# Kernel tuning notes

Measured on AMD Instinct MI355X. Metric: run time of the kernel, lower is better.

The kernel has to match this reference:

```python
import jax, jax.numpy as jnp
import numpy as np

DIM = 1024
BATCH = 8
SEQ = 2048


def setup_inputs() -> dict:
    key = jax.random.key(0)
    ks = jax.random.split(key, 10)
    s = 0.02
    return {
        "x": jax.random.normal(ks[0], (BATCH, SEQ, DIM), dtype=jnp.float32),
        "Wq": jax.random.normal(ks[1], (DIM, DIM), dtype=jnp.float32) * s,
        "bq": jnp.zeros((DIM,), jnp.float32),
        "Wk": jax.random.normal(ks[2], (DIM, DIM), dtype=jnp.float32) * s,
        "bk": jnp.zeros((DIM,), jnp.float32),
        "Wv": jax.random.normal(ks[3], (DIM, DIM), dtype=jnp.float32) * s,
        "bv": jnp.zeros((DIM,), jnp.float32),
        "Wo": jax.random.normal(ks[4], (DIM, DIM), dtype=jnp.float32) * s,
        "bo": jnp.zeros((DIM,), jnp.float32),
        "decay_param": jnp.asarray(0.0, jnp.float32),
    }


def reference(x, Wq, bq, Wk, bk, Wv, bv, Wo, bo, decay_param):
    # projections: [B,S,D] @ [D,D]
    q = x @ Wq + bq
    k = jax.nn.elu(x @ Wk + bk) + 1.0  # F.elu(k) + 1.0
    v = x @ Wv + bv
    decay = jax.nn.sigmoid(decay_param)
    B, S, D = x.shape

    def step(mem, qkv):
        q_t, k_t, v_t = qkv  # each [B, D]
        # read BEFORE update (output at t uses memory from steps < t)
        read = jnp.einsum('bd,bde->be', q_t, mem)
        mem = decay * mem + k_t[:, :, None] * v_t[:, None, :]  # rank-1 outer product
        return mem, read

    mem0 = jnp.zeros((B, D, D), x.dtype)
    # scan over time: move seq axis to front
    _, outs = jax.lax.scan(
        step, mem0,
        (q.transpose(1, 0, 2), k.transpose(1, 0, 2), v.transpose(1, 0, 2)))
    out = outs.transpose(1, 0, 2)  # [B, S, D]
    return out @ Wo + bo
```

## Files before the change

kernel.cpp:

```cpp
#include <hip/hip_runtime.h>
#include <cstdint>
#include <cstddef>

typedef __bf16 bf16;
typedef __attribute__((ext_vector_type(8))) __bf16 bf16x8;
typedef __attribute__((ext_vector_type(4))) __bf16 bf16x4;
typedef __attribute__((ext_vector_type(4))) float f32x4;
typedef __attribute__((ext_vector_type(4))) int i32x4;

#define ADIM 1024
#define ASEQ 2048
#define ABATCH 8

__device__ __forceinline__ void gload_lds16(const void* g, void* l) {
  __builtin_amdgcn_global_load_lds(
      (const __attribute__((address_space(1))) void*)g,
      (__attribute__((address_space(3))) void*)l,
      16, 0, 0);
}

__device__ __forceinline__ f32x4 mfma16(bf16x8 a, bf16x8 b, f32x4 c) {
  return __builtin_amdgcn_mfma_f32_16x16x32_bf16(a, b, c, 0, 0, 0);
}
__device__ __forceinline__ i32x4 mfma8i(i32x4 a, i32x4 b, i32x4 c) {
  return __builtin_amdgcn_mfma_i32_16x16x64_i8(a, b, c, 0, 0, 0);
}

__global__ __launch_bounds__(256) void k_prep_w(
    const float* __restrict__ Wq, const float* __restrict__ Wk,
    const float* __restrict__ Wv, const float* __restrict__ Wo,
    bf16* __restrict__ WcT, bf16* __restrict__ WoT) {
  const int b = blockIdx.x;
  const int which = b >> 8, t = b & 255;
  const int n0 = (t & 15) * 64, k0 = (t >> 4) * 64;
  const float* W = (which == 0) ? Wq : (which == 1) ? Wk : (which == 2) ? Wv : Wo;
  bf16* out = (which < 3) ? (WcT + (size_t)which * ADIM * ADIM) : WoT;

  __shared__ float tile[64][69];
  const int r = threadIdx.x >> 4, c4 = (threadIdx.x & 15) * 4;
#pragma unroll
  for (int p = 0; p < 4; ++p) {
    float4 f = *(const float4*)&W[(size_t)(k0 + p * 16 + r) * ADIM + n0 + c4];
    tile[p * 16 + r][c4 + 0] = f.x;
    tile[p * 16 + r][c4 + 1] = f.y;
    tile[p * 16 + r][c4 + 2] = f.z;
    tile[p * 16 + r][c4 + 3] = f.w;
  }
  __syncthreads();
#pragma unroll
  for (int p = 0; p < 4; ++p) {
    const int nn = p * 16 + r;
    bf16x4 o;
#pragma unroll
    for (int j = 0; j < 4; ++j) o[j] = (bf16)tile[c4 + j][nn];
    *(bf16x4*)&out[(size_t)(n0 + nn) * ADIM + k0 + c4] = o;
  }
}

__global__ __launch_bounds__(256) void k_q(
    const float* __restrict__ x, const bf16* __restrict__ WcT,
    signed char* __restrict__ Xq, float* __restrict__ sx,
    signed char* __restrict__ WcQ, float* __restrict__ swc) {
  const int row = blockIdx.x * 4 + (threadIdx.x >> 6);
  const int l = threadIdx.x & 63;
  float v[16];
  if (row < 16384) {
    const float4* p = (const float4*)&x[(size_t)row * ADIM + l * 16];
#pragma unroll
    for (int g = 0; g < 4; ++g) {
      float4 f = p[g];
      v[g * 4 + 0] = f.x; v[g * 4 + 1] = f.y; v[g * 4 + 2] = f.z; v[g * 4 + 3] = f.w;
    }
  } else {
    const bf16x8* p = (const bf16x8*)&WcT[(size_t)(row - 16384) * ADIM + l * 16];
#pragma unroll
    for (int g = 0; g < 2; ++g) {
      bf16x8 f = p[g];
#pragma unroll
      for (int e = 0; e < 8; ++e) v[g * 8 + e] = (float)f[e];
    }
  }
  float m = 0.f;
#pragma unroll
  for (int e = 0; e < 16; ++e) m = fmaxf(m, fabsf(v[e]));
#pragma unroll
  for (int off = 32; off >= 1; off >>= 1) m = fmaxf(m, __shfl_xor(m, off));
  m = fmaxf(m, 1e-20f);
  const float inv = 127.f / m;
  i32x4 pk;
#pragma unroll
  for (int g = 0; g < 4; ++g) {
    int word = 0;
#pragma unroll
    for (int e = 0; e < 4; ++e) {
      int q = __float2int_rn(v[g * 4 + e] * inv);
      q = max(-127, min(127, q));
      word |= (q & 255) << (e * 8);
    }
    pk[g] = word;
  }
  if (row < 16384) {
    *(i32x4*)&Xq[(size_t)row * ADIM + l * 16] = pk;
    if (l == 0) sx[row] = m / 127.f;
  } else {
    *(i32x4*)&WcQ[(size_t)(row - 16384) * ADIM + l * 16] = pk;
    if (l == 0) swc[row - 16384] = m / 127.f;
  }
}

__global__ __launch_bounds__(512, 2) void k_qkv8(
    const signed char* __restrict__ A, const signed char* __restrict__ BT,
    const float* __restrict__ sx, const float* __restrict__ swc,
    const float* __restrict__ bias0, const float* __restrict__ bias1,
    const float* __restrict__ bias2,
    bf16* __restrict__ Qo, bf16* __restrict__ Ko, bf16* __restrict__ Vto)
{
  constexpr int K = 1024;
  constexpr int KT = 16;
  const int nwg = gridDim.x;
  const int cpx = nwg >> 3;
  const int flat = blockIdx.x;
  const int sw = (flat & 7) * cpx + (flat >> 3);
  const int bx = sw % 12, by = sw / 12;
  const int m0 = by * 256, n0 = bx * 256;

  const int tid = threadIdx.x;
  const int l = tid & 63, w = tid >> 6;
  const int wm = w >> 2, wn = w & 3;
  const int lr = l & 15, kg = l >> 4;

  __shared__ alignas(16) signed char sA[3][256 * 64];
  __shared__ alignas(16) signed char sB[3][256 * 64];

  i32x4 acc[8][4] = {};

  int oA[8], oB[4];
#pragma unroll
  for (int i = 0; i < 8; ++i) {
    int r = wm * 128 + i * 16 + lr;
    oA[i] = (r * 4 + (kg ^ (r & 3))) * 16;
  }
#pragma unroll
  for (int j = 0; j < 4; ++j) {
    int r = wn * 64 + j * 16 + lr;
    oB[j] = (r * 4 + (kg ^ (r & 3))) * 16;
  }

  auto stA = [&](int sp, int kt, int chunk) {
    int s = chunk * 512 + tid;
    int prow = s >> 2, ps = s & 3;
    int lc = ps ^ (prow & 3);
    gload_lds16(A + (size_t)(m0 + prow) * K + kt * 64 + lc * 16,
                &sA[sp][(size_t)s * 16]);
  };
  auto stB = [&](int sp, int kt, int chunk) {
    int s = chunk * 512 + tid;
    int prow = s >> 2, ps = s & 3;
    int lc = ps ^ (prow & 3);
    gload_lds16(BT + (size_t)(n0 + prow) * K + kt * 64 + lc * 16,
                &sB[sp][(size_t)s * 16]);
  };

#pragma unroll
  for (int tt = 0; tt < 2; ++tt) {
    stA(tt, tt, 0); stA(tt, tt, 1);
    stB(tt, tt, 0); stB(tt, tt, 1);
  }
  asm volatile("s_waitcnt vmcnt(4)\n\ts_barrier" ::: "memory");

  for (int t = 0; t < KT; ++t) {
    const int s = t % 3;
    const char* bA = (const char*)&sA[s][0];
    const char* bB = (const char*)&sB[s][0];

    i32x4 af[8], bfr[4];
#pragma unroll
    for (int i = 0; i < 8; ++i) af[i] = *(const i32x4*)(bA + oA[i]);
#pragma unroll
    for (int j = 0; j < 4; ++j) bfr[j] = *(const i32x4*)(bB + oB[j]);

    const int tp = (t + 2 < KT) ? t + 2 : t;
    stA((t + 2) % 3, tp, 0); stA((t + 2) % 3, tp, 1);
    stB((t + 2) % 3, tp, 0); stB((t + 2) % 3, tp, 1);

    __builtin_amdgcn_s_setprio(1);
#pragma unroll
    for (int i = 0; i < 8; ++i)
#pragma unroll
      for (int j = 0; j < 4; ++j)
        acc[i][j] = mfma8i(af[i], bfr[j], acc[i][j]);
    __builtin_amdgcn_s_setprio(0);

    asm volatile("s_waitcnt vmcnt(4)\n\ts_barrier" ::: "memory");
  }
  asm volatile("s_waitcnt vmcnt(0)" ::: "memory");

  const int cb = n0 >> 10;
#pragma unroll
  for (int i = 0; i < 8; ++i) {
#pragma unroll
    for (int jj = 0; jj < 4; ++jj) {
      const int n = n0 + wn * 64 + jj * 16 + lr;
      const int m0r = m0 + wm * 128 + i * 16 + kg * 4;
      const int nn = n & 1023;
      const float swn = swc[n];
      const float4 s4 = *(const float4*)&sx[m0r];
      float de[4];
      de[0] = (float)acc[i][jj][0] * s4.x * swn;
      de[1] = (float)acc[i][jj][1] * s4.y * swn;
      de[2] = (float)acc[i][jj][2] * s4.z * swn;
      de[3] = (float)acc[i][jj][3] * s4.w * swn;
      if (cb == 0) {
        const float b_ = bias0[nn];
#pragma unroll
        for (int r = 0; r < 4; ++r)
          Qo[(size_t)(m0r + r) * ADIM + nn] = (bf16)(de[r] + b_);
      } else if (cb == 1) {
        const float b_ = bias1[nn];
#pragma unroll
        for (int r = 0; r < 4; ++r) {
          float v = de[r] + b_;
          Ko[(size_t)(m0r + r) * ADIM + nn] = (bf16)(v > 0.f ? v + 1.f : __expf(v));
        }
      } else {
        const float b_ = bias2[nn];
        const int bb = m0r >> 11, t0c = m0r & 2047;
        bf16x4 pk;
#pragma unroll
        for (int r = 0; r < 4; ++r) pk[r] = (bf16)(de[r] + b_);
        *(bf16x4*)&Vto[((size_t)bb * ADIM + nn) * ASEQ + t0c] = pk;
      }
    }
  }
}

__global__ __launch_bounds__(512, 2) void k_gout(
    const bf16* __restrict__ A, const bf16* __restrict__ BT,
    const float* __restrict__ bias0, float* __restrict__ outF)
{
  constexpr int K = 1024;
  constexpr int KT = 16;
  const int nwg = gridDim.x;
  const int cpx = nwg >> 3;
  const int flat = blockIdx.x;
  const int sw = (flat & 7) * cpx + (flat >> 3);
  const int bx = sw % 4, by = sw / 4;
  const int m0 = by * 256, n0 = bx * 256;

  const int tid = threadIdx.x;
  const int l = tid & 63, w = tid >> 6;
  const int wm = w >> 2, wn = w & 3;
  const int lr = l & 15, kg = l >> 4;

  __shared__ alignas(16) bf16 sA[2][256 * 64];
  __shared__ alignas(16) bf16 sB[2][256 * 64];

  f32x4 acc[8][4] = {};

  int oA[8], oB[4];
#pragma unroll
  for (int i = 0; i < 8; ++i) {
    int r = wm * 128 + i * 16 + lr;
    oA[i] = (r * 8 + (kg ^ (r & 7))) * 16;
  }
#pragma unroll
  for (int j = 0; j < 4; ++j) {
    int r = wn * 64 + j * 16 + lr;
    oB[j] = (r * 8 + (kg ^ (r & 7))) * 16;
  }

  auto stA = [&](int c, int kt, int chunk) {
    int s = chunk * 512 + tid;
    int prow = s >> 3, ps = s & 7;
    int lc = ps ^ (prow & 7);
    gload_lds16(A + (size_t)(m0 + prow) * K + kt * 64 + lc * 8,
                &sA[c][(size_t)s * 8]);
  };
  auto stB = [&](int c, int kt, int chunk) {
    int s = chunk * 512 + tid;
    int prow = s >> 3, ps = s & 7;
    int lc = ps ^ (prow & 7);
    gload_lds16(BT + (size_t)(n0 + prow) * K + kt * 64 + lc * 8,
                &sB[c][(size_t)s * 8]);
  };

#pragma unroll
  for (int ch = 0; ch < 4; ++ch) { stA(0, 0, ch); stB(0, 0, ch); }
  asm volatile("s_waitcnt vmcnt(0)\n\ts_barrier" ::: "memory");

  for (int t = 0; t < KT; ++t) {
    const int c = t & 1;
    const char* bA = (const char*)&sA[c][0];
    const char* bB = (const char*)&sB[c][0];

    bf16x8 af[8], bfr[4];
#pragma unroll
    for (int i = 0; i < 8; ++i) af[i] = *(const bf16x8*)(bA + oA[i]);
#pragma unroll
    for (int j = 0; j < 4; ++j) bfr[j] = *(const bf16x8*)(bB + oB[j]);

    if (t + 1 < KT) {
#pragma unroll
      for (int ch = 0; ch < 4; ++ch) { stA(c ^ 1, t + 1, ch); stB(c ^ 1, t + 1, ch); }
    }

    __builtin_amdgcn_s_setprio(1);
#pragma unroll
    for (int i = 0; i < 8; ++i)
#pragma unroll
      for (int j = 0; j < 4; ++j)
        acc[i][j] = mfma16(af[i], bfr[j], acc[i][j]);
    __builtin_amdgcn_s_setprio(0);

#pragma unroll
    for (int i = 0; i < 8; ++i) af[i] = *(const bf16x8*)(bA + (oA[i] ^ 64));
#pragma unroll
    for (int j = 0; j < 4; ++j) bfr[j] = *(const bf16x8*)(bB + (oB[j] ^ 64));

    __builtin_amdgcn_s_setprio(1);
#pragma unroll
    for (int i = 0; i < 8; ++i)
#pragma unroll
      for (int j = 0; j < 4; ++j)
        acc[i][j] = mfma16(af[i], bfr[j], acc[i][j]);
    __builtin_amdgcn_s_setprio(0);

    asm volatile("s_waitcnt vmcnt(0)\n\ts_barrier" ::: "memory");
  }

#pragma unroll
  for (int i = 0; i < 8; ++i) {
#pragma unroll
    for (int jj = 0; jj < 4; ++jj) {
      const int n = n0 + wn * 64 + jj * 16 + lr;
      const int m0r = m0 + wm * 128 + i * 16 + kg * 4;
      const float b_ = bias0[n];
#pragma unroll
      for (int r = 0; r < 4; ++r)
        outF[(size_t)(m0r + r) * ADIM + n] = acc[i][jj][r] + b_;
    }
  }
}

__global__ __launch_bounds__(256) void k_attn(
    const bf16* __restrict__ Qg, const bf16* __restrict__ Kg,
    const bf16* __restrict__ Vt, bf16* __restrict__ Rb,
    const float* __restrict__ decay_param)
{
  const int b = blockIdx.y;
  const int T0 = blockIdx.x * 64;
  const int tid = threadIdx.x;
  const int l = tid & 63, w = tid >> 6;
  const int lr = l & 15, lk = (l >> 4) * 8;

  const float dp = decay_param[0];
  const float decay = 1.f / (1.f + __expf(-dp));
  const float l2d = __log2f(decay);

  __shared__ alignas(16) bf16 lQ[3][64 * 32];
  __shared__ alignas(16) bf16 lK[3][128 * 32];
  __shared__ alignas(16) bf16 lV[3][128 * 32];
  __shared__ alignas(16) bf16 lP[64 * 136];

  const bf16* Qb = Qg + (size_t)(b * ASEQ + T0) * ADIM;

  auto stageQK = [&](int buf, int k0) {
    {
      const bf16* g = Qb + (size_t)(w * 16 + (l >> 2)) * ADIM + k0 + (l & 3) * 8;
      gload_lds16(g, &lQ[buf][w * 16 * 32]);
    }
#pragma unroll
    for (int cc = 0; cc < 2; ++cc) {
      int c = 2 * w + cc;
      int sg = T0 - 64 + c * 16 + (l >> 2);
      if (sg < 0) sg = 0;
      const bf16* g = Kg + (size_t)(b * ASEQ + sg) * ADIM + k0 + (l & 3) * 8;
      gload_lds16(g, &lK[buf][c * 16 * 32]);
    }
  };

  f32x4 sc[4][2] = {};
  stageQK(0, 0);
  stageQK(1, 32);
  asm volatile("s_waitcnt vmcnt(3)\n\ts_barrier" ::: "memory");

  for (int kt = 0; kt < 32; ++kt) {
    const int cur = kt % 3;
    bf16x8 af[4], bfr[2];
#pragma unroll
    for (int i = 0; i < 4; ++i)
      af[i] = *(const bf16x8*)&lQ[cur][(i * 16 + lr) * 32 + lk];
#pragma unroll
    for (int j = 0; j < 2; ++j)
      bfr[j] = *(const bf16x8*)&lK[cur][(w * 32 + j * 16 + lr) * 32 + lk];

    const int tp = (kt + 2 < 32) ? kt + 2 : kt;
    stageQK((kt + 2) % 3, tp * 32);

#pragma unroll
    for (int i = 0; i < 4; ++i)
#pragma unroll
      for (int j = 0; j < 2; ++j)
        sc[i][j] = mfma16(af[i], bfr[j], sc[i][j]);

    asm volatile("s_waitcnt vmcnt(3)\n\ts_barrier" ::: "memory");
  }

  const int er = (l >> 4) * 4, ec = l & 15;
#pragma unroll
  for (int i = 0; i < 4; ++i)
#pragma unroll
    for (int j = 0; j < 2; ++j)
#pragma unroll
      for (int r = 0; r < 4; ++r) {
        int tl = i * 16 + er + r;
        int sl = w * 32 + j * 16 + ec;
        int sg = T0 - 64 + sl;
        int delta = (T0 + tl) - 1 - sg;
        float wgt = (delta >= 0 && delta < 64 && sg >= 0)
                        ? exp2f((float)delta * l2d) : 0.f;
        lP[tl * 136 + sl] = (bf16)(sc[i][j][r] * wgt);
      }

  auto stageV = [&](int buf, int g) {
    int nc = g >> 2, ks = g & 3;
#pragma unroll
    for (int cc = 0; cc < 2; ++cc) {
      int c = 2 * w + cc;
      int drow = nc * 128 + c * 16 + (l >> 2);
      int scol = T0 - 64 + ks * 32 + (l & 3) * 8;
      if (scol < 0) scol = 0;
      const bf16* gv = Vt + ((size_t)b * ADIM + drow) * ASEQ + scol;
      gload_lds16(gv, &lV[buf][c * 16 * 32]);
    }
  };

  stageV(0, 0);
  stageV(1, 1);
  asm volatile("s_waitcnt vmcnt(2) lgkmcnt(0)\n\ts_barrier" ::: "memory");

  f32x4 o[4][2] = {};
  for (int g = 0; g < 32; ++g) {
    const int cur = g % 3;
    const int nc = g >> 2, ks = g & 3;
    bf16x8 af[4], bfr[2];
#pragma unroll
    for (int i = 0; i < 4; ++i)
      af[i] = *(const bf16x8*)&lP[(i * 16 + lr) * 136 + ks * 32 + lk];
#pragma unroll
    for (int j = 0; j < 2; ++j)
      bfr[j] = *(const bf16x8*)&lV[cur][(w * 32 + j * 16 + lr) * 32 + lk];

    const int gp = (g + 2 < 32) ? g + 2 : g;
    stageV((g + 2) % 3, gp);

#pragma unroll
    for (int i = 0; i < 4; ++i)
#pragma unroll
      for (int j = 0; j < 2; ++j)
        o[i][j] = mfma16(af[i], bfr[j], o[i][j]);

    if (ks == 3) {
#pragma unroll
      for (int i = 0; i < 4; ++i)
#pragma unroll
        for (int j = 0; j < 2; ++j) {
#pragma unroll
          for (int r = 0; r < 4; ++r) {
            int tl = i * 16 + er + r;
            int dl = nc * 128 + w * 32 + j * 16 + ec;
            Rb[(size_t)(b * ASEQ + T0 + tl) * ADIM + dl] = (bf16)o[i][j][r];
          }
#pragma unroll
          for (int r = 0; r < 4; ++r) o[i][j][r] = 0.f;
        }
    }
    asm volatile("s_waitcnt vmcnt(2)\n\ts_barrier" ::: "memory");
  }
  asm volatile("s_waitcnt vmcnt(0)" ::: "memory");
}

extern "C" void kernel_launch(void* const* d_in, const int* in_sizes, int n_in,
                              void* d_out, int out_size, void* d_ws, size_t ws_size,
                              hipStream_t stream) {
  const float* x  = (const float*)d_in[0];
  const float* Wq = (const float*)d_in[1];
  const float* bq = (const float*)d_in[2];
  const float* Wk = (const float*)d_in[3];
  const float* bk = (const float*)d_in[4];
  const float* Wv = (const float*)d_in[5];
  const float* bv = (const float*)d_in[6];
  const float* Wo = (const float*)d_in[7];
  const float* bo = (const float*)d_in[8];
  const float* dp = (const float*)d_in[9];
  float* out = (float*)d_out;

  char* ws = (char*)d_ws;
  signed char* Xq  = (signed char*)(ws + ((size_t)0 << 20));
  float*       sx  = (float*)(ws + ((size_t)16 << 20));
  signed char* WcQ = (signed char*)(ws + ((size_t)17 << 20));
  float*       swc = (float*)(ws + ((size_t)20 << 20));
  bf16* Qb  = (bf16*)(ws + ((size_t)32 << 20));
  bf16* Kb  = (bf16*)(ws + ((size_t)64 << 20));
  bf16* Vtb = (bf16*)(ws + ((size_t)96 << 20));
  bf16* Rbb = (bf16*)(ws + ((size_t)128 << 20));
  bf16* WcT = (bf16*)(ws + ((size_t)160 << 20));
  bf16* WoT = (bf16*)(ws + ((size_t)166 << 20));

  k_prep_w<<<1024, 256, 0, stream>>>(Wq, Wk, Wv, Wo, WcT, WoT);
  k_q<<<4864, 256, 0, stream>>>(x, WcT, Xq, sx, WcQ, swc);
  k_qkv8<<<768, 512, 0, stream>>>(
      Xq, WcQ, sx, swc, bq, bk, bv, Qb, Kb, Vtb);
  k_attn<<<dim3(32, 8), 256, 0, stream>>>(Qb, Kb, Vtb, Rbb, dp);
  k_gout<<<256, 512, 0, stream>>>(Rbb, WoT, bo, out);
}
```

Before: 182.5 us.

## Quantize output projection to int8 and unify GEMMs with BK=128 double-buffered kernel

Quantizes the attention read output and Wo to int8 with per-row scales and runs the output projection with int8 MFMA instead of bf16. This adds a separate quantization kernel for R. Both GEMMs now share one templated kernel that uses 128-wide K tiles with double buffering, replacing the QKV GEMM's 64-wide triple-buffered pipeline. This trades an extra pass over R and lower output precision for cheaper MFMA and less operand bandwidth in the final GEMM.

Measured after the change: 176.2 us. 3.5% less time.

```diff
diff --git a/kernel.cpp b/kernel.cpp
--- a/kernel.cpp
+++ b/kernel.cpp
@@ -59,8 +59,10 @@
 
 __global__ __launch_bounds__(256) void k_q(
     const float* __restrict__ x, const bf16* __restrict__ WcT,
+    const bf16* __restrict__ WoT,
     signed char* __restrict__ Xq, float* __restrict__ sx,
-    signed char* __restrict__ WcQ, float* __restrict__ swc) {
+    signed char* __restrict__ WcQ, float* __restrict__ swc,
+    signed char* __restrict__ WoQ, float* __restrict__ swo) {
   const int row = blockIdx.x * 4 + (threadIdx.x >> 6);
   const int l = threadIdx.x & 63;
   float v[16];
@@ -72,7 +74,10 @@
       v[g * 4 + 0] = f.x; v[g * 4 + 1] = f.y; v[g * 4 + 2] = f.z; v[g * 4 + 3] = f.w;
     }
   } else {
-    const bf16x8* p = (const bf16x8*)&WcT[(size_t)(row - 16384) * ADIM + l * 16];
+    const bf16* src = (row < 19456)
+        ? (WcT + (size_t)(row - 16384) * ADIM)
+        : (WoT + (size_t)(row - 19456) * ADIM);
+    const bf16x8* p = (const bf16x8*)&src[l * 16];
 #pragma unroll
     for (int g = 0; g < 2; ++g) {
       bf16x8 f = p[g];
@@ -102,26 +107,67 @@
   if (row < 16384) {
     *(i32x4*)&Xq[(size_t)row * ADIM + l * 16] = pk;
     if (l == 0) sx[row] = m / 127.f;
-  } else {
+  } else if (row < 19456) {
     *(i32x4*)&WcQ[(size_t)(row - 16384) * ADIM + l * 16] = pk;
     if (l == 0) swc[row - 16384] = m / 127.f;
-  }
-}
-
-__global__ __launch_bounds__(512, 2) void k_qkv8(
+  } else {
+    *(i32x4*)&WoQ[(size_t)(row - 19456) * ADIM + l * 16] = pk;
+    if (l == 0) swo[row - 19456] = m / 127.f;
+  }
+}
+
+__global__ __launch_bounds__(256) void k_qr(
+    const bf16* __restrict__ Rb, signed char* __restrict__ Rq,
+    float* __restrict__ sxr) {
+  const int row = blockIdx.x * 4 + (threadIdx.x >> 6);
+  const int l = threadIdx.x & 63;
+  float v[16];
+  const bf16x8* p = (const bf16x8*)&Rb[(size_t)row * ADIM + l * 16];
+#pragma unroll
+  for (int g = 0; g < 2; ++g) {
+    bf16x8 f = p[g];
+#pragma unroll
+    for (int e = 0; e < 8; ++e) v[g * 8 + e] = (float)f[e];
+  }
+  float m = 0.f;
+#pragma unroll
+  for (int e = 0; e < 16; ++e) m = fmaxf(m, fabsf(v[e]));
+#pragma unroll
+  for (int off = 32; off >= 1; off >>= 1) m = fmaxf(m, __shfl_xor(m, off));
+  m = fmaxf(m, 1e-20f);
+  const float inv = 127.f / m;
+  i32x4 pk;
+#pragma unroll
+  for (int g = 0; g < 4; ++g) {
+    int word = 0;
+#pragma unroll
+    for (int e = 0; e < 4; ++e) {
+      int q = __float2int_rn(v[g * 4 + e] * inv);
+      q = max(-127, min(127, q));
+      word |= (q & 255) << (e * 8);
+    }
+    pk[g] = word;
+  }
+  *(i32x4*)&Rq[(size_t)row * ADIM + l * 16] = pk;
+  if (l == 0) sxr[row] = m / 127.f;
+}
+
+template<int MODE>
+__global__ __launch_bounds__(512, 2) void k_gi8(
     const signed char* __restrict__ A, const signed char* __restrict__ BT,
-    const float* __restrict__ sx, const float* __restrict__ swc,
+    const float* __restrict__ sa, const float* __restrict__ sb,
     const float* __restrict__ bias0, const float* __restrict__ bias1,
     const float* __restrict__ bias2,
-    bf16* __restrict__ Qo, bf16* __restrict__ Ko, bf16* __restrict__ Vto)
+    bf16* __restrict__ Qo, bf16* __restrict__ Ko, bf16* __restrict__ Vto,
+    float* __restrict__ outF, int ntn)
 {
   constexpr int K = 1024;
-  constexpr int KT = 16;
+  constexpr int KT = 8;
   const int nwg = gridDim.x;
   const int cpx = nwg >> 3;
   const int flat = blockIdx.x;
   const int sw = (flat & 7) * cpx + (flat >> 3);
-  const int bx = sw % 12, by = sw / 12;
+  const int bx = sw % ntn, by = sw / ntn;
   const int m0 = by * 256, n0 = bx * 256;
 
   const int tid = threadIdx.x;
@@ -129,133 +175,10 @@
   const int wm = w >> 2, wn = w & 3;
   const int lr = l & 15, kg = l >> 4;
 
-  __shared__ alignas(16) signed char sA[3][256 * 64];
-  __shared__ alignas(16) signed char sB[3][256 * 64];
+  __shared__ alignas(16) signed char sA[2][256 * 128];
+  __shared__ alignas(16) signed char sB[2][256 * 128];
 
   i32x4 acc[8][4] = {};
-
-  int oA[8], oB[4];
-#pragma unroll
-  for (int i = 0; i < 8; ++i) {
-    int r = wm * 128 + i * 16 + lr;
-    oA[i] = (r * 4 + (kg ^ (r & 3))) * 16;
-  }
-#pragma unroll
-  for (int j = 0; j < 4; ++j) {
-    int r = wn * 64 + j * 16 + lr;
-    oB[j] = (r * 4 + (kg ^ (r & 3))) * 16;
-  }
-
-  auto stA = [&](int sp, int kt, int chunk) {
-    int s = chunk * 512 + tid;
-    int prow = s >> 2, ps = s & 3;
-    int lc = ps ^ (prow & 3);
-    gload_lds16(A + (size_t)(m0 + prow) * K + kt * 64 + lc * 16,
-                &sA[sp][(size_t)s * 16]);
-  };
-  auto stB = [&](int sp, int kt, int chunk) {
-    int s = chunk * 512 + tid;
-    int prow = s >> 2, ps = s & 3;
-    int lc = ps ^ (prow & 3);
-    gload_lds16(BT + (size_t)(n0 + prow) * K + kt * 64 + lc * 16,
-                &sB[sp][(size_t)s * 16]);
-  };
-
-#pragma unroll
-  for (int tt = 0; tt < 2; ++tt) {
-    stA(tt, tt, 0); stA(tt, tt, 1);
-    stB(tt, tt, 0); stB(tt, tt, 1);
-  }
-  asm volatile("s_waitcnt vmcnt(4)\n\ts_barrier" ::: "memory");
-
-  for (int t = 0; t < KT; ++t) {
-    const int s = t % 3;
-    const char* bA = (const char*)&sA[s][0];
-    const char* bB = (const char*)&sB[s][0];
-
-    i32x4 af[8], bfr[4];
-#pragma unroll
-    for (int i = 0; i < 8; ++i) af[i] = *(const i32x4*)(bA + oA[i]);
-#pragma unroll
-    for (int j = 0; j < 4; ++j) bfr[j] = *(const i32x4*)(bB + oB[j]);
-
-    const int tp = (t + 2 < KT) ? t + 2 : t;
-    stA((t + 2) % 3, tp, 0); stA((t + 2) % 3, tp, 1);
-    stB((t + 2) % 3, tp, 0); stB((t + 2) % 3, tp, 1);
-
-    __builtin_amdgcn_s_setprio(1);
-#pragma unroll
-    for (int i = 0; i < 8; ++i)
-#pragma unroll
-      for (int j = 0; j < 4; ++j)
-        acc[i][j] = mfma8i(af[i], bfr[j], acc[i][j]);
-    __builtin_amdgcn_s_setprio(0);
-
-    asm volatile("s_waitcnt vmcnt(4)\n\ts_barrier" ::: "memory");
-  }
-  asm volatile("s_waitcnt vmcnt(0)" ::: "memory");
-
-  const int cb = n0 >> 10;
-#pragma unroll
-  for (int i = 0; i < 8; ++i) {
-#pragma unroll
-    for (int jj = 0; jj < 4; ++jj) {
-      const int n = n0 + wn * 64 + jj * 16 + lr;
-      const int m0r = m0 + wm * 128 + i * 16 + kg * 4;
-      const int nn = n & 1023;
-      const float swn = swc[n];
-      const float4 s4 = *(const float4*)&sx[m0r];
-      float de[4];
-      de[0] = (float)acc[i][jj][0] * s4.x * swn;
-      de[1] = (float)acc[i][jj][1] * s4.y * swn;
-      de[2] = (float)acc[i][jj][2] * s4.z * swn;
-      de[3] = (float)acc[i][jj][3] * s4.w * swn;
-      if (cb == 0) {
-        const float b_ = bias0[nn];
-#pragma unroll
-        for (int r = 0; r < 4; ++r)
-          Qo[(size_t)(m0r + r) * ADIM + nn] = (bf16)(de[r] + b_);
-      } else if (cb == 1) {
-        const float b_ = bias1[nn];
-#pragma unroll
-        for (int r = 0; r < 4; ++r) {
-          float v = de[r] + b_;
-          Ko[(size_t)(m0r + r) * ADIM + nn] = (bf16)(v > 0.f ? v + 1.f : __expf(v));
-        }
-      } else {
-        const float b_ = bias2[nn];
-        const int bb = m0r >> 11, t0c = m0r & 2047;
-        bf16x4 pk;
-#pragma unroll
-        for (int r = 0; r < 4; ++r) pk[r] = (bf16)(de[r] + b_);
-        *(bf16x4*)&Vto[((size_t)bb * ADIM + nn) * ASEQ + t0c] = pk;
-      }
-    }
-  }
-}
-
-__global__ __launch_bounds__(512, 2) void k_gout(
-    const bf16* __restrict__ A, const bf16* __restrict__ BT,
-    const float* __restrict__ bias0, float* __restrict__ outF)
-{
-  constexpr int K = 1024;
-  constexpr int KT = 16;
-  const int nwg = gridDim.x;
-  const int cpx = nwg >> 3;
-  const int flat = blockIdx.x;
-  const int sw = (flat & 7) * cpx + (flat >> 3);
-  const int bx = sw % 4, by = sw / 4;
-  const int m0 = by * 256, n0 = bx * 256;
-
-  const int tid = threadIdx.x;
-  const int l = tid & 63, w = tid >> 6;
-  const int wm = w >> 2, wn = w & 3;
-  const int lr = l & 15, kg = l >> 4;
-
-  __shared__ alignas(16) bf16 sA[2][256 * 64];
-  __shared__ alignas(16) bf16 sB[2][256 * 64];
-
-  f32x4 acc[8][4] = {};
 
   int oA[8], oB[4];
 #pragma unroll
@@ -273,15 +196,15 @@
     int s = chunk * 512 + tid;
     int prow = s >> 3, ps = s & 7;
     int lc = ps ^ (prow & 7);
-    gload_lds16(A + (size_t)(m0 + prow) * K + kt * 64 + lc * 8,
-                &sA[c][(size_t)s * 8]);
+    gload_lds16(A + (size_t)(m0 + prow) * K + kt * 128 + lc * 16,
+                &sA[c][(size_t)s * 16]);
   };
   auto stB = [&](int c, int kt, int chunk) {
     int s = chunk * 512 + tid;
     int prow = s >> 3, ps = s & 7;
     int lc = ps ^ (prow & 7);
-    gload_lds16(BT + (size_t)(n0 + prow) * K + kt * 64 + lc * 8,
-                &sB[c][(size_t)s * 8]);
+    gload_lds16(BT + (size_t)(n0 + prow) * K + kt * 128 + lc * 16,
+                &sB[c][(size_t)s * 16]);
   };
 
 #pragma unroll
@@ -293,11 +216,11 @@
     const char* bA = (const char*)&sA[c][0];
     const char* bB = (const char*)&sB[c][0];
 
-    bf16x8 af[8], bfr[4];
-#pragma unroll
-    for (int i = 0; i < 8; ++i) af[i] = *(const bf16x8*)(bA + oA[i]);
-#pragma unroll
-    for (int j = 0; j < 4; ++j) bfr[j] = *(const bf16x8*)(bB + oB[j]);
+    i32x4 af[8], bfr[4];
+#pragma unroll
+    for (int i = 0; i < 8; ++i) af[i] = *(const i32x4*)(bA + oA[i]);
+#pragma unroll
+    for (int j = 0; j < 4; ++j) bfr[j] = *(const i32x4*)(bB + oB[j]);
 
     if (t + 1 < KT) {
 #pragma unroll
@@ -309,35 +232,67 @@
     for (int i = 0; i < 8; ++i)
 #pragma unroll
       for (int j = 0; j < 4; ++j)
-        acc[i][j] = mfma16(af[i], bfr[j], acc[i][j]);
+        acc[i][j] = mfma8i(af[i], bfr[j], acc[i][j]);
     __builtin_amdgcn_s_setprio(0);
 
 #pragma unroll
-    for (int i = 0; i < 8; ++i) af[i] = *(const bf16x8*)(bA + (oA[i] ^ 64));
-#pragma unroll
-    for (int j = 0; j < 4; ++j) bfr[j] = *(const bf16x8*)(bB + (oB[j] ^ 64));
+    for (int i = 0; i < 8; ++i) af[i] = *(const i32x4*)(bA + (oA[i] ^ 64));
+#pragma unroll
+    for (int j = 0; j < 4; ++j) bfr[j] = *(const i32x4*)(bB + (oB[j] ^ 64));
 
     __builtin_amdgcn_s_setprio(1);
 #pragma unroll
     for (int i = 0; i < 8; ++i)
 #pragma unroll
       for (int j = 0; j < 4; ++j)
-        acc[i][j] = mfma16(af[i], bfr[j], acc[i][j]);
+        acc[i][j] = mfma8i(af[i], bfr[j], acc[i][j]);
     __builtin_amdgcn_s_setprio(0);
 
     asm volatile("s_waitcnt vmcnt(0)\n\ts_barrier" ::: "memory");
   }
 
+  const int cb = n0 >> 10;
 #pragma unroll
   for (int i = 0; i < 8; ++i) {
 #pragma unroll
     for (int jj = 0; jj < 4; ++jj) {
       const int n = n0 + wn * 64 + jj * 16 + lr;
       const int m0r = m0 + wm * 128 + i * 16 + kg * 4;
-      const float b_ = bias0[n];
-#pragma unroll
-      for (int r = 0; r < 4; ++r)
-        outF[(size_t)(m0r + r) * ADIM + n] = acc[i][jj][r] + b_;
+      const float sbn = sb[n];
+      const float4 s4 = *(const float4*)&sa[m0r];
+      float de[4];
+      de[0] = (float)acc[i][jj][0] * s4.x * sbn;
+      de[1] = (float)acc[i][jj][1] * s4.y * sbn;
+      de[2] = (float)acc[i][jj][2] * s4.z * sbn;
+      de[3] = (float)acc[i][jj][3] * s4.w * sbn;
+      if (MODE == 0) {
+        const int nn = n & 1023;
+        if (cb == 0) {
+          const float b_ = bias0[nn];
+#pragma unroll
+          for (int r = 0; r < 4; ++r)
+            Qo[(size_t)(m0r + r) * ADIM + nn] = (bf16)(de[r] + b_);
+        } else if (cb == 1) {
+          const float b_ = bias1[nn];
+#pragma unroll
+          for (int r = 0; r < 4; ++r) {
+            float v = de[r] + b_;
+            Ko[(size_t)(m0r + r) * ADIM + nn] = (bf16)(v > 0.f ? v + 1.f : __expf(v));
+          }
+        } else {
+          const float b_ = bias2[nn];
+          const int bb = m0r >> 11, t0c = m0r & 2047;
+          bf16x4 pk;
+#pragma unroll
+          for (int r = 0; r < 4; ++r) pk[r] = (bf16)(de[r] + b_);
+          *(bf16x4*)&Vto[((size_t)bb * ADIM + nn) * ASEQ + t0c] = pk;
+        }
+      } else {
+        const float b_ = bias0[n];
+#pragma unroll
+        for (int r = 0; r < 4; ++r)
+          outF[(size_t)(m0r + r) * ADIM + n] = de[r] + b_;
+      }
     }
   }
 }
@@ -497,9 +452,13 @@
 
   char* ws = (char*)d_ws;
   signed char* Xq  = (signed char*)(ws + ((size_t)0 << 20));
+  signed char* Rq  = Xq;
   float*       sx  = (float*)(ws + ((size_t)16 << 20));
+  float*       sxr = sx;
   signed char* WcQ = (signed char*)(ws + ((size_t)17 << 20));
   float*       swc = (float*)(ws + ((size_t)20 << 20));
+  signed char* WoQ = (signed char*)(ws + ((size_t)21 << 20));
+  float*       swo = (float*)(ws + ((size_t)22 << 20));
   bf16* Qb  = (bf16*)(ws + ((size_t)32 << 20));
   bf16* Kb  = (bf16*)(ws + ((size_t)64 << 20));
   bf16* Vtb = (bf16*)(ws + ((size_t)96 << 20));
@@ -508,9 +467,11 @@
   bf16* WoT = (bf16*)(ws + ((size_t)166 << 20));
 
   k_prep_w<<<1024, 256, 0, stream>>>(Wq, Wk, Wv, Wo, WcT, WoT);
-  k_q<<<4864, 256, 0, stream>>>(x, WcT, Xq, sx, WcQ, swc);
-  k_qkv8<<<768, 512, 0, stream>>>(
-      Xq, WcQ, sx, swc, bq, bk, bv, Qb, Kb, Vtb);
+  k_q<<<5120, 256, 0, stream>>>(x, WcT, WoT, Xq, sx, WcQ, swc, WoQ, swo);
+  k_gi8<0><<<768, 512, 0, stream>>>(
+      Xq, WcQ, sx, swc, bq, bk, bv, Qb, Kb, Vtb, nullptr, 12);
   k_attn<<<dim3(32, 8), 256, 0, stream>>>(Qb, Kb, Vtb, Rbb, dp);
-  k_gout<<<256, 512, 0, stream>>>(Rbb, WoT, bo, out);
-}
+  k_qr<<<4096, 256, 0, stream>>>(Rbb, Rq, sxr);
+  k_gi8<1><<<256, 512, 0, stream>>>(
+      Rq, WoQ, sxr, swo, bo, nullptr, nullptr, nullptr, nullptr, nullptr, out, 4);
+}
```
